# Kernel tuning notes

Measured on AMD Instinct MI355X. Metric: run time of the kernel, lower is better.

The kernel has to match this reference:

```python
import jax, jax.numpy as jnp
import numpy as np

N_NODES = 200000
IN_DIM = 128
HID = 64
WALK_LEN = 16          # max_step + 1
NUM_WALKS = 16         # = hidden_graphs, walks per graph
N_GRAPHS = 1024
PEN = 32
N_CLASSES = 10
BN_EPS = 1e-5


def setup_inputs() -> dict:
    key = jax.random.key(0)
    ks = jax.random.split(key, 16)
    x = jax.random.normal(ks[0], (N_NODES, IN_DIM), dtype=jnp.float32)
    walks = jax.random.randint(ks[1], (N_GRAPHS * NUM_WALKS, WALK_LEN), 0, N_NODES)
    # each graph contributes NUM_WALKS consecutive walks
    walk_batch = jnp.repeat(jnp.arange(N_GRAPHS), NUM_WALKS)
    s = 1.0 / np.sqrt(HID)
    return {
        "x": x,
        "walks": walks,
        "walk_batch": walk_batch,
        "W_enc": jax.random.normal(ks[2], (HID, IN_DIM), jnp.float32) / np.sqrt(IN_DIM),
        "b_enc": jnp.zeros((HID,), jnp.float32),
        "W_ih": jax.random.uniform(ks[3], (3 * HID, HID), jnp.float32, -s, s),
        "W_hh": jax.random.uniform(ks[4], (3 * HID, HID), jnp.float32, -s, s),
        "b_ih": jax.random.uniform(ks[5], (3 * HID,), jnp.float32, -s, s),
        "b_hh": jax.random.uniform(ks[6], (3 * HID,), jnp.float32, -s, s),
        "gamma": jnp.ones((HID,), jnp.float32),
        "beta": jnp.zeros((HID,), jnp.float32),
        "W1": jax.random.normal(ks[7], (PEN, HID), jnp.float32) / np.sqrt(HID),
        "b1": jnp.zeros((PEN,), jnp.float32),
        "W2": jax.random.normal(ks[8], (N_CLASSES, PEN), jnp.float32) / np.sqrt(PEN),
        "b2": jnp.zeros((N_CLASSES,), jnp.float32),
    }


def _gru_cell(h, xt, W_ih, W_hh, b_ih, b_hh):
    # PyTorch GRU gate math
    gi = xt @ W_ih.T + b_ih            # [W, 3H]
    gh = h @ W_hh.T + b_hh             # [W, 3H]
    i_r, i_z, i_n = jnp.split(gi, 3, axis=-1)
    h_r, h_z, h_n = jnp.split(gh, 3, axis=-1)
    r = jax.nn.sigmoid(i_r + h_r)
    z = jax.nn.sigmoid(i_z + h_z)
    n = jnp.tanh(i_n + r * h_n)
    return (1.0 - z) * n + z * h


def reference(x, walks, walk_batch, W_enc, b_enc, W_ih, W_hh, b_ih, b_hh,
              gamma, beta, W1, b1, W2, b2):
    # feature encoder on all nodes, then gather along walks
    x_enc = x @ W_enc.T + b_enc                     # [N, H]
    walk_feats = x_enc[walks]                       # [W, L, H] gather
    xs = jnp.swapaxes(walk_feats, 0, 1)             # [L, W, H]

    def step(h, xt):
        return _gru_cell(h, xt, W_ih, W_hh, b_ih, b_hh), None

    h0 = jnp.zeros((walks.shape[0], HID), walk_feats.dtype)
    h_final, _ = jax.lax.scan(step, h0, xs)         # [W, H] last hidden state

    # segment-mean pooling per graph
    seg_sum = jax.ops.segment_sum(h_final, walk_batch, num_segments=N_GRAPHS)
    cnt = jax.ops.segment_sum(jnp.ones((walks.shape[0],), h_final.dtype),
                              walk_batch, num_segments=N_GRAPHS)
    graph_enc = seg_sum / jnp.maximum(cnt, 1.0)[:, None]   # [B, H]

    # BatchNorm1d (training mode: batch statistics, biased variance)
    mean = jnp.mean(graph_enc, axis=0)
    var = jnp.mean(jnp.square(graph_enc - mean), axis=0)
    gn = (graph_enc - mean) / jnp.sqrt(var + BN_EPS) * gamma + beta

    h1 = jax.nn.relu(gn @ W1.T + b1)                # dropout p=0 -> identity
    logits = h1 @ W2.T + b2
    return jax.nn.log_softmax(logits, axis=1)
```

## Files before the change

kernel.cpp:

```cpp
#include <hip/hip_runtime.h>

typedef _Float16 half8 __attribute__((ext_vector_type(8)));
typedef _Float16 half4 __attribute__((ext_vector_type(4)));
typedef float f32x4 __attribute__((ext_vector_type(4)));

#define MFMA_F16(A, B, C) __builtin_amdgcn_mfma_f32_16x16x32_f16(A, B, C, 0, 0, 0)

#define NN 200000

__device__ __forceinline__ half8 cvt8(const float* p) {
  half8 a;
#pragma unroll
  for (int e = 0; e < 8; ++e) a[e] = (_Float16)p[e];
  return a;
}

__global__ __launch_bounds__(256, 2) void k_enc(const float* __restrict__ x,
                                                const float* __restrict__ Wenc,
                                                const float* __restrict__ benc,
                                                _Float16* __restrict__ xenc) {
  __shared__ _Float16 wlds[16 * 64 * 8];

  const int tid = threadIdx.x;
  const int lane = tid & 63, wv = tid >> 6;
  const int r = lane & 15, g = lane >> 4;

  for (int i4 = tid; i4 < 2048; i4 += 256) {
    int idx = i4 * 4;
    f32x4 v = *(const f32x4*)(Wenc + idx);
    int j = idx >> 7, k = idx & 127;
    int tile = (j >> 4) * 4 + (k >> 5);
    int ln = ((k >> 3) & 3) * 16 + (j & 15);
    half4 h;
    h[0] = (_Float16)v[0]; h[1] = (_Float16)v[1];
    h[2] = (_Float16)v[2]; h[3] = (_Float16)v[3];
    *(half4*)&wlds[(tile * 64 + ln) * 8 + (k & 7)] = h;
  }
  __syncthreads();

  half8 W[4][4];
#pragma unroll
  for (int jt = 0; jt < 4; ++jt)
#pragma unroll
    for (int kt = 0; kt < 4; ++kt)
      W[jt][kt] = *(const half8*)&wlds[((jt * 4 + kt) * 64 + lane) * 8];

  float bb[4][4];
#pragma unroll
  for (int jt = 0; jt < 4; ++jt)
#pragma unroll
    for (int rr = 0; rr < 4; ++rr) bb[jt][rr] = benc[jt * 16 + g * 4 + rr];

  const int base = blockIdx.x * 256 + wv * 64;

  f32x4 xr[4][4][2];
#pragma unroll
  for (int mt = 0; mt < 4; ++mt) {
    int arow = base + mt * 16 + r;
    if (arow >= NN) arow = NN - 1;
    const float* rowp = x + (size_t)arow * 128;
#pragma unroll
    for (int kt = 0; kt < 4; ++kt) {
      const f32x4* p = (const f32x4*)(rowp + kt * 32 + g * 8);
      xr[mt][kt][0] = p[0];
      xr[mt][kt][1] = p[1];
    }
  }

#pragma unroll
  for (int mt = 0; mt < 4; ++mt) {
    f32x4 acc[4];
#pragma unroll
    for (int jt = 0; jt < 4; ++jt)
      acc[jt] = (f32x4){bb[jt][0], bb[jt][1], bb[jt][2], bb[jt][3]};

#pragma unroll
    for (int kt = 0; kt < 4; ++kt) {
      half8 a;
#pragma unroll
      for (int e = 0; e < 4; ++e) {
        a[e] = (_Float16)xr[mt][kt][0][e];
        a[4 + e] = (_Float16)xr[mt][kt][1][e];
      }
#pragma unroll
      for (int jt = 0; jt < 4; ++jt)
        acc[jt] = MFMA_F16(W[jt][kt], a, acc[jt]);
    }

    int node = base + mt * 16 + r;
    if (node < NN) {
#pragma unroll
      for (int jt = 0; jt < 4; ++jt) {
        half4 o;
        o[0] = (_Float16)acc[jt][0]; o[1] = (_Float16)acc[jt][1];
        o[2] = (_Float16)acc[jt][2]; o[3] = (_Float16)acc[jt][3];
        *(half4*)&xenc[(size_t)node * 64 + jt * 16 + g * 4] = o;
      }
    }
  }
}

__global__ __launch_bounds__(256, 1) void k_gru(const _Float16* __restrict__ xenc,
                                                const int* __restrict__ walks,
                                                const float* __restrict__ Wih,
                                                const float* __restrict__ Whh,
                                                const float* __restrict__ bih,
                                                const float* __restrict__ bhh,
                                                float* __restrict__ genc) {
  __shared__ _Float16 h_lds[4][16 * 64];
  __shared__ int ids[4][256];

  const int tid = threadIdx.x;
  const int lane = tid & 63, wv = tid >> 6;
  const int r = lane & 15, g = lane >> 4;

  half8 Bih[12][2], Bhh[12][2];
#pragma unroll
  for (int jt = 0; jt < 12; ++jt)
#pragma unroll
    for (int kt = 0; kt < 2; ++kt) {
      Bih[jt][kt] = cvt8(Wih + (jt * 16 + r) * 64 + kt * 32 + g * 8);
      Bhh[jt][kt] = cvt8(Whh + (jt * 16 + r) * 64 + kt * 32 + g * 8);
    }

  float brz[8], bin4[4], bhn4[4];
#pragma unroll
  for (int jt = 0; jt < 8; ++jt) brz[jt] = bih[jt * 16 + r] + bhh[jt * 16 + r];
#pragma unroll
  for (int jt = 0; jt < 4; ++jt) {
    bin4[jt] = bih[128 + jt * 16 + r];
    bhn4[jt] = bhh[128 + jt * 16 + r];
  }

  const int gph = blockIdx.x * 4 + wv;
  {
    const int* wp = walks + gph * 256;
    int4 v = *(const int4*)(wp + lane * 4);
    int vals[4] = {v.x, v.y, v.z, v.w};
#pragma unroll
    for (int i = 0; i < 4; ++i) {
      int m = lane * 4 + i;
      ids[wv][(m & 15) * 16 + (m >> 4)] = vals[i];
    }
  }

  for (int i = lane; i < 16 * 64; i += 64) h_lds[wv][i] = (_Float16)0.f;

  f32x4 h[4];
#pragma unroll
  for (int jt = 0; jt < 4; ++jt) h[jt] = (f32x4){0.f, 0.f, 0.f, 0.f};

  char* hbase = (char*)&h_lds[wv][0];
  const int swz = (r & 7) << 4;

  int nid0 = ids[wv][r];
  const _Float16* xp0 = xenc + (size_t)nid0 * 64 + g * 8;
  half8 Ax0 = *(const half8*)xp0;
  half8 Ax1 = *(const half8*)(xp0 + 32);

#pragma unroll 2
  for (int t = 0; t < 16; ++t) {
    int tn = (t + 1) & 15;
    int nid = ids[wv][tn * 16 + r];
    const _Float16* xp = xenc + (size_t)nid * 64 + g * 8;
    half8 Nx0 = *(const half8*)xp;
    half8 Nx1 = *(const half8*)(xp + 32);

    half8 Ah0 = *(const half8*)(hbase + ((r * 128 + g * 16) ^ swz));
    half8 Ah1 = *(const half8*)(hbase + ((r * 128 + 64 + g * 16) ^ swz));

    f32x4 aRZ[8], aIN[4], aHN[4];
#pragma unroll
    for (int jt = 0; jt < 8; ++jt) aRZ[jt] = (f32x4){brz[jt], brz[jt], brz[jt], brz[jt]};
#pragma unroll
    for (int jt = 0; jt < 4; ++jt) {
      aIN[jt] = (f32x4){bin4[jt], bin4[jt], bin4[jt], bin4[jt]};
      aHN[jt] = (f32x4){bhn4[jt], bhn4[jt], bhn4[jt], bhn4[jt]};
    }

#pragma unroll
    for (int jt = 0; jt < 8; ++jt) {
      aRZ[jt] = MFMA_F16(Ax0, Bih[jt][0], aRZ[jt]);
      aRZ[jt] = MFMA_F16(Ax1, Bih[jt][1], aRZ[jt]);
    }
#pragma unroll
    for (int jt = 0; jt < 4; ++jt) {
      aIN[jt] = MFMA_F16(Ax0, Bih[8 + jt][0], aIN[jt]);
      aIN[jt] = MFMA_F16(Ax1, Bih[8 + jt][1], aIN[jt]);
    }

#pragma unroll
    for (int jt = 0; jt < 8; ++jt) {
      aRZ[jt] = MFMA_F16(Ah0, Bhh[jt][0], aRZ[jt]);
      aRZ[jt] = MFMA_F16(Ah1, Bhh[jt][1], aRZ[jt]);
    }
#pragma unroll
    for (int jt = 0; jt < 4; ++jt) {
      aHN[jt] = MFMA_F16(Ah0, Bhh[8 + jt][0], aHN[jt]);
      aHN[jt] = MFMA_F16(Ah1, Bhh[8 + jt][1], aHN[jt]);
    }

#pragma unroll
    for (int jt = 0; jt < 4; ++jt)
#pragma unroll
      for (int rr = 0; rr < 4; ++rr) {
        float pr = aRZ[jt][rr];
        float pz = aRZ[4 + jt][rr];
        float rg = __builtin_amdgcn_rcpf(1.f + __expf(-pr));
        float zg = __builtin_amdgcn_rcpf(1.f + __expf(-pz));
        float pn = aIN[jt][rr] + rg * aHN[jt][rr];
        float e2 = __expf(2.f * pn);
        float nn = 1.f - 2.f * __builtin_amdgcn_rcpf(e2 + 1.f);
        h[jt][rr] = (1.f - zg) * nn + zg * h[jt][rr];
      }

    if (t < 15) {
#pragma unroll
      for (int jt = 0; jt < 4; ++jt)
#pragma unroll
        for (int rr = 0; rr < 4; ++rr) {
          int row = g * 4 + rr;
          int byte = (row * 128 + (jt * 16 + r) * 2) ^ ((row & 7) << 4);
          *(_Float16*)(hbase + byte) = (_Float16)h[jt][rr];
        }
    }

    Ax0 = Nx0;
    Ax1 = Nx1;
  }

#pragma unroll
  for (int jt = 0; jt < 4; ++jt) {
    float s = h[jt][0] + h[jt][1] + h[jt][2] + h[jt][3];
    s += __shfl_xor(s, 16);
    s += __shfl_xor(s, 32);
    if (g == 0) genc[gph * 64 + jt * 16 + r] = s * 0.0625f;
  }
}

__global__ __launch_bounds__(1024) void k_stats(const float* __restrict__ genc,
                                                const float* __restrict__ gamma,
                                                const float* __restrict__ beta,
                                                float* __restrict__ ss) {
  __shared__ float sum_s[16][64], sq_s[16][64];
  int j = threadIdx.x & 63, grp = threadIdx.x >> 6;
  float s = 0.f, q = 0.f;
#pragma unroll 4
  for (int rr = 0; rr < 64; ++rr) {
    float v = genc[(grp * 64 + rr) * 64 + j];
    s += v;
    q += v * v;
  }
  sum_s[grp][j] = s;
  sq_s[grp][j] = q;
  __syncthreads();
  if (grp == 0) {
    float S = 0.f, Q = 0.f;
#pragma unroll
    for (int k = 0; k < 16; ++k) {
      S += sum_s[k][j];
      Q += sq_s[k][j];
    }
    float mean = S * (1.f / 1024.f);
    float var = Q * (1.f / 1024.f) - mean * mean;
    float rstd = rsqrtf(var + 1e-5f);
    float sc = gamma[j] * rstd;
    ss[j] = sc;
    ss[64 + j] = beta[j] - mean * sc;
  }
}

__global__ __launch_bounds__(256, 1) void k_mlp(const float* __restrict__ genc,
                                                const float* __restrict__ ss,
                                                const float* __restrict__ W1,
                                                const float* __restrict__ b1,
                                                const float* __restrict__ W2,
                                                const float* __restrict__ b2,
                                                float* __restrict__ out) {
  __shared__ float w1[32 * 64], w2[10 * 32], bb1[32], bb2[10], sc[64], sh[64];
  const int tid = threadIdx.x;
  for (int i = tid; i < 32 * 64; i += 256) w1[i] = W1[i];
  for (int i = tid; i < 10 * 32; i += 256) w2[i] = W2[i];
  if (tid < 32) bb1[tid] = b1[tid];
  if (tid >= 32 && tid < 42) bb2[tid - 32] = b2[tid - 32];
  if (tid >= 64 && tid < 128) sc[tid - 64] = ss[tid - 64];
  if (tid >= 128 && tid < 192) sh[tid - 128] = ss[64 + tid - 128];
  __syncthreads();

  const int row = blockIdx.x * 256 + tid;
  float gn[64];
  const f32x4* gp = (const f32x4*)(genc + row * 64);
#pragma unroll
  for (int jq = 0; jq < 16; ++jq) {
    f32x4 v = gp[jq];
#pragma unroll
    for (int e = 0; e < 4; ++e) gn[jq * 4 + e] = v[e] * sc[jq * 4 + e] + sh[jq * 4 + e];
  }

  float h1[32];
#pragma unroll
  for (int i = 0; i < 32; ++i) {
    float a = bb1[i];
#pragma unroll
    for (int j = 0; j < 64; ++j) a += w1[i * 64 + j] * gn[j];
    h1[i] = fmaxf(a, 0.f);
  }

  float lg[10];
  float mx = -1e30f;
#pragma unroll
  for (int c = 0; c < 10; ++c) {
    float a = bb2[c];
#pragma unroll
    for (int i = 0; i < 32; ++i) a += w2[c * 32 + i] * h1[i];
    lg[c] = a;
    mx = fmaxf(mx, a);
  }
  float se = 0.f;
#pragma unroll
  for (int c = 0; c < 10; ++c) se += __expf(lg[c] - mx);
  float lse = mx + __logf(se);
#pragma unroll
  for (int c = 0; c < 10; ++c) out[row * 10 + c] = lg[c] - lse;
}

extern "C" void kernel_launch(void* const* d_in, const int* in_sizes, int n_in,
                              void* d_out, int out_size, void* d_ws, size_t ws_size,
                              hipStream_t stream) {
  const float* x = (const float*)d_in[0];
  const int* walks = (const int*)d_in[1];
  const float* Wenc = (const float*)d_in[3];
  const float* benc = (const float*)d_in[4];
  const float* Wih = (const float*)d_in[5];
  const float* Whh = (const float*)d_in[6];
  const float* bih = (const float*)d_in[7];
  const float* bhh = (const float*)d_in[8];
  const float* gamma = (const float*)d_in[9];
  const float* beta = (const float*)d_in[10];
  const float* W1 = (const float*)d_in[11];
  const float* b1 = (const float*)d_in[12];
  const float* W2 = (const float*)d_in[13];
  const float* b2 = (const float*)d_in[14];
  float* out = (float*)d_out;

  char* ws = (char*)d_ws;
  _Float16* xenc = (_Float16*)ws;
  float* genc = (float*)(ws + 25600000);
  float* ss = (float*)(ws + 25600000 + 262144);

  k_enc<<<dim3(782), dim3(256), 0, stream>>>(x, Wenc, benc, xenc);
  k_gru<<<dim3(256), dim3(256), 0, stream>>>(xenc, walks, Wih, Whh, bih, bhh, genc);
  k_stats<<<dim3(1), dim3(1024), 0, stream>>>(genc, gamma, beta, ss);
  k_mlp<<<dim3(4), dim3(256), 0, stream>>>(genc, ss, W1, b1, W2, b2, out);
}
```

Baseline: 100.2 us.

## Stage encoder input rows into LDS via direct global-to-LDS loads

The encoder kernel now copies a 128-row tile of x straight into swizzled shared memory using global_load_lds 16-byte transfers, then reads MFMA operands from LDS instead of holding 32 float4 registers per thread. The tile per block is halved and the grid doubled, so more blocks are in flight with lower register pressure. This aims at better coalescing and latency hiding for the bandwidth-bound read of x (about 100 MB). In exchange it uses 64 KB of LDS per block, which may cap occupancy, and the weight setup is repeated in twice as many blocks.

Result: no change. 101.0 us (+0.7%).

```diff
diff --git a/kernel.cpp b/kernel.cpp
--- a/kernel.cpp
+++ b/kernel.cpp
@@ -1,4 +1,5 @@
 #include <hip/hip_runtime.h>
+#include <stdint.h>
 
 typedef _Float16 half8 __attribute__((ext_vector_type(8)));
 typedef _Float16 half4 __attribute__((ext_vector_type(4)));
@@ -13,17 +14,36 @@
 #pragma unroll
   for (int e = 0; e < 8; ++e) a[e] = (_Float16)p[e];
   return a;
+}
+
+__device__ __forceinline__ void gload_lds16(const void* gp, void* lp) {
+  __builtin_amdgcn_global_load_lds(
+      (const __attribute__((address_space(1))) uint32_t*)(gp),
+      (__attribute__((address_space(3))) uint32_t*)(lp), 16, 0, 0);
 }
 
 __global__ __launch_bounds__(256, 2) void k_enc(const float* __restrict__ x,
                                                 const float* __restrict__ Wenc,
                                                 const float* __restrict__ benc,
                                                 _Float16* __restrict__ xenc) {
+  __shared__ float xl[128 * 128];
   __shared__ _Float16 wlds[16 * 64 * 8];
 
   const int tid = threadIdx.x;
   const int lane = tid & 63, wv = tid >> 6;
   const int r = lane & 15, g = lane >> 4;
+  const int base = blockIdx.x * 128;
+
+#pragma unroll
+  for (int i = 0; i < 16; ++i) {
+    int row = wv * 32 + 2 * i + (lane >> 5);
+    int grow = base + row;
+    if (grow >= NN) grow = NN - 1;
+    int scol = ((lane & 31) * 16) ^ ((row & 7) << 4);
+    const char* gp = (const char*)(x + (size_t)grow * 128) + scol;
+    char* lp = (char*)xl + (wv * 32 + 2 * i) * 512;
+    gload_lds16(gp, lp);
+  }
 
   for (int i4 = tid; i4 < 2048; i4 += 256) {
     int idx = i4 * 4;
@@ -36,6 +56,7 @@
     h[2] = (_Float16)v[2]; h[3] = (_Float16)v[3];
     *(half4*)&wlds[(tile * 64 + ln) * 8 + (k & 7)] = h;
   }
+
   __syncthreads();
 
   half8 W[4][4];
@@ -51,24 +72,13 @@
 #pragma unroll
     for (int rr = 0; rr < 4; ++rr) bb[jt][rr] = benc[jt * 16 + g * 4 + rr];
 
-  const int base = blockIdx.x * 256 + wv * 64;
-
-  f32x4 xr[4][4][2];
-#pragma unroll
-  for (int mt = 0; mt < 4; ++mt) {
-    int arow = base + mt * 16 + r;
-    if (arow >= NN) arow = NN - 1;
-    const float* rowp = x + (size_t)arow * 128;
-#pragma unroll
-    for (int kt = 0; kt < 4; ++kt) {
-      const f32x4* p = (const f32x4*)(rowp + kt * 32 + g * 8);
-      xr[mt][kt][0] = p[0];
-      xr[mt][kt][1] = p[1];
-    }
-  }
-
-#pragma unroll
-  for (int mt = 0; mt < 4; ++mt) {
+  const int sw = (r & 7) << 4;
+
+#pragma unroll
+  for (int mt = 0; mt < 2; ++mt) {
+    const int row = wv * 32 + mt * 16 + r;
+    const char* rp = (const char*)xl + row * 512;
+
     f32x4 acc[4];
 #pragma unroll
     for (int jt = 0; jt < 4; ++jt)
@@ -76,18 +86,20 @@
 
 #pragma unroll
     for (int kt = 0; kt < 4; ++kt) {
+      f32x4 v0 = *(const f32x4*)(rp + ((kt * 128 + g * 32) ^ sw));
+      f32x4 v1 = *(const f32x4*)(rp + ((kt * 128 + g * 32 + 16) ^ sw));
       half8 a;
 #pragma unroll
       for (int e = 0; e < 4; ++e) {
-        a[e] = (_Float16)xr[mt][kt][0][e];
-        a[4 + e] = (_Float16)xr[mt][kt][1][e];
+        a[e] = (_Float16)v0[e];
+        a[4 + e] = (_Float16)v1[e];
       }
 #pragma unroll
       for (int jt = 0; jt < 4; ++jt)
         acc[jt] = MFMA_F16(W[jt][kt], a, acc[jt]);
     }
 
-    int node = base + mt * 16 + r;
+    int node = base + wv * 32 + mt * 16 + r;
     if (node < NN) {
 #pragma unroll
       for (int jt = 0; jt < 4; ++jt) {
@@ -348,7 +360,7 @@
   float* genc = (float*)(ws + 25600000);
   float* ss = (float*)(ws + 25600000 + 262144);
 
-  k_enc<<<dim3(782), dim3(256), 0, stream>>>(x, Wenc, benc, xenc);
+  k_enc<<<dim3(1563), dim3(256), 0, stream>>>(x, Wenc, benc, xenc);
   k_gru<<<dim3(256), dim3(256), 0, stream>>>(xenc, walks, Wih, Whh, bih, bhh, genc);
   k_stats<<<dim3(1), dim3(1024), 0, stream>>>(genc, gamma, beta, ss);
   k_mlp<<<dim3(4), dim3(256), 0, stream>>>(genc, ss, W1, b1, W2, b2, out);
```
